# Kernel optimization log

Measured on AMD Instinct MI355X. Metric: run time of the kernel, lower is better.

The kernel has to match this reference:

```python
import jax, jax.numpy as jnp
import numpy as np

AH, AW = 7, 7                # aligned_height, aligned_width
SPATIAL_SCALE = 0.0625       # 1/16


def setup_inputs() -> dict:
    key = jax.random.key(0)
    k1, k2, k3, k4 = jax.random.split(key, 4)
    B, C, H, W = 4, 1024, 64, 64
    N = 2048
    IMG = 1024.0  # image size in pixels; IMG * SPATIAL_SCALE == W
    features = jax.random.normal(k1, (B, C, H, W), dtype=jnp.float32)
    bidx = jax.random.randint(k2, (N,), 0, B).astype(jnp.float32)
    xy1 = jax.random.uniform(k3, (N, 2), minval=0.0, maxval=IMG * 0.7)
    wh = jax.random.uniform(k4, (N, 2), minval=16.0, maxval=IMG * 0.3)
    xy2 = jnp.minimum(xy1 + wh, IMG - 1.0)
    rois = jnp.concatenate(
        [bidx[:, None], xy1[:, 0:1], xy1[:, 1:2], xy2[:, 0:1], xy2[:, 1:2]], axis=1
    ).astype(jnp.float32)
    return {"features": features, "rois": rois}


def reference(features, rois):
    # Faithful port of jwyang's roi_align_kernel (1 sample per bin, inclusive
    # endpoint grid: bin_size = roi_extent / (aligned - 1)).
    B, C, H, W = features.shape
    N = rois.shape[0]
    dt = features.dtype

    batch_ind = rois[:, 0].astype(jnp.int32)                      # [N]
    x1 = rois[:, 1] * SPATIAL_SCALE
    y1 = rois[:, 2] * SPATIAL_SCALE
    x2 = rois[:, 3] * SPATIAL_SCALE
    y2 = rois[:, 4] * SPATIAL_SCALE

    roi_w = jnp.maximum(x2 - x1, 0.0)
    roi_h = jnp.maximum(y2 - y1, 0.0)
    bin_w = roi_w / (AW - 1.0)
    bin_h = roi_h / (AH - 1.0)

    ph = jnp.arange(AH, dtype=dt)
    pw = jnp.arange(AW, dtype=dt)
    h = y1[:, None] + ph[None, :] * bin_h[:, None]                # [N, AH]
    w = x1[:, None] + pw[None, :] * bin_w[:, None]                # [N, AW]

    hstart = jnp.minimum(jnp.floor(h), H - 2.0)                   # [N, AH]
    wstart = jnp.minimum(jnp.floor(w), W - 2.0)                   # [N, AW]
    h_ratio = h - hstart                                          # [N, AH]
    w_ratio = w - wstart                                          # [N, AW]

    # Kernel zeroes out-of-bounds samples.
    valid = ((h >= 0) & (h < H))[:, :, None] & ((w >= 0) & (w < W))[:, None, :]

    hs = jnp.clip(hstart.astype(jnp.int32), 0, H - 2)             # safe gather idx
    ws = jnp.clip(wstart.astype(jnp.int32), 0, W - 2)

    b = batch_ind[:, None, None]                                  # [N,1,1]
    hi = hs[:, :, None]                                           # [N,AH,1]
    wi = ws[:, None, :]                                           # [N,1,AW]

    def gather(dh, dw):
        # mixed advanced indexing -> [N, AH, AW, C]
        return features[b, :, hi + dh, wi + dw]

    ul, ur = gather(0, 0), gather(0, 1)
    dl, dr = gather(1, 0), gather(1, 1)

    hr = h_ratio[:, :, None, None]                                # [N,AH,1,1]
    wr = w_ratio[:, None, :, None]                                # [N,1,AW,1]
    out = (ul * (1 - hr) * (1 - wr) + ur * (1 - hr) * wr
           + dl * hr * (1 - wr) + dr * hr * wr)                   # [N,AH,AW,C]
    out = jnp.where(valid[..., None], out, 0.0)
    return jnp.transpose(out, (0, 3, 1, 2))                       # [N,C,AH,AW]
```

## Files before the change

kernel.cpp:

```cpp
#include <hip/hip_runtime.h>


#define SCALE    0.0625f
#define C_       1024
#define H_       64
#define W_       64
#define HW       (H_ * W_)
#define CHW      (C_ * HW)
#define AH_      7
#define AW_      7
#define NBIN     49
#define PER_ROI  (C_ * NBIN)
#define QCH      32
#define NSLICE   (C_ / QCH)
#define CHUNK    8
#define RCAP     14
#define QCAP     8
#define CSPAN    36
#define NXCD     8

__global__ __launch_bounds__(256, 8) void roialign_kernel(
    const float* __restrict__ feat,
    const float* __restrict__ rois,
    float* __restrict__ out,
    int N)
{
    __shared__ __align__(16) float s_data[CHUNK][RCAP * CSPAN];
    __shared__ float4 s_w[NBIN];
    __shared__ int    s_hs[NBIN], s_ws[NBIN];
    __shared__ int    s_ul[NBIN], s_dl[NBIN];
    __shared__ int    s_goff[NBIN];
    __shared__ int    s_rowG[RCAP];
    __shared__ int    s_quadG[16];
    __shared__ int    s_R, s_Q, s_b;

    const unsigned bidx = blockIdx.x;
    const int xcd       = (int)(bidx & (NXCD - 1));
    const unsigned tmp  = bidx >> 3;
    const int roi       = (int)(tmp % (unsigned)N);
    const int slice_sub = (int)(tmp / (unsigned)N);
    const int slice     = slice_sub * NXCD + xcd;
    const int t = threadIdx.x;

    unsigned long long rm = 0ull;
    unsigned int       qm = 0u;

    if (t < 64) {
        int hs = 0, ws = 0;
        if (t < NBIN) {
            #pragma clang fp contract(off)
            const float r0 = rois[roi * 5 + 0];
            const float r1 = rois[roi * 5 + 1];
            const float r2 = rois[roi * 5 + 2];
            const float r3 = rois[roi * 5 + 3];
            const float r4 = rois[roi * 5 + 4];
            const int   b  = (int)r0;
            const float x1 = r1 * SCALE;
            const float y1 = r2 * SCALE;
            const float x2 = r3 * SCALE;
            const float y2 = r4 * SCALE;
            const float roi_w = fmaxf(x2 - x1, 0.0f);
            const float roi_h = fmaxf(y2 - y1, 0.0f);
            const float bin_w = roi_w / (float)(AW_ - 1);
            const float bin_h = roi_h / (float)(AH_ - 1);

            const int ph = t / AW_;
            const int pw = t - ph * AW_;

            const float h = y1 + (float)ph * bin_h;
            const float w = x1 + (float)pw * bin_w;

            const float hstart = fminf(floorf(h), (float)(H_ - 2));
            const float wstart = fminf(floorf(w), (float)(W_ - 2));
            const float hr = h - hstart;
            const float wr = w - wstart;

            const bool valid = (h >= 0.0f) && (h < (float)H_) &&
                               (w >= 0.0f) && (w < (float)W_);

            hs = min(max((int)hstart, 0), H_ - 2);
            ws = min(max((int)wstart, 0), W_ - 2);

            float wul = (1.0f - hr) * (1.0f - wr);
            float wur = (1.0f - hr) * wr;
            float wdl = hr * (1.0f - wr);
            float wdr = hr * wr;
            if (!valid) { wul = 0.0f; wur = 0.0f; wdl = 0.0f; wdr = 0.0f; }

            s_w[t]    = make_float4(wul, wur, wdl, wdr);
            s_hs[t]   = hs;
            s_ws[t]   = ws;
            s_goff[t] = hs * W_ + ws;
            if (t == 0) s_b = b;

            rm = 3ull << hs;
            qm = (1u << (ws >> 2)) | (1u << ((ws + 1) >> 2));
        }

        #pragma unroll
        for (int d = 1; d < 64; d <<= 1) {
            rm |= __shfl_xor(rm, d);
            qm |= __shfl_xor(qm, d);
        }

        if ((rm >> t) & 1ull)
            s_rowG[__popcll(rm & ((1ull << t) - 1ull))] = t;
        if (t < 16 && ((qm >> t) & 1u))
            s_quadG[__popc(qm & ((1u << t) - 1u))] = t;
        if (t == 0) { s_R = (int)__popcll(rm); s_Q = __popc(qm); }

        if (t < NBIN) {
            const int colIdx = 4 * __popc(qm & ((1u << (ws >> 2)) - 1u)) + (ws & 3);
            const int rsu = __popcll(rm & ((1ull << hs) - 1ull));
            const int rsd = __popcll(rm & ((2ull << hs) - 1ull));
            s_ul[t] = rsu * CSPAN + colIdx;
            s_dl[t] = rsd * CSPAN + colIdx;
        }
    }
    __syncthreads();

    const int R  = s_R;
    const int Qn = s_Q;
    const int rq = R * Qn;

    const float* featC = feat + (size_t)s_b * CHW + (size_t)(slice * QCH) * HW;
    float*       ob    = out + (size_t)roi * PER_ROI + (size_t)(slice * QCH) * NBIN;

    if (Qn > QCAP || R > RCAP) {
        for (int e = t; e < QCH * NBIN; e += 256) {
            const unsigned eu  = (unsigned)e;
            const unsigned c   = eu / NBIN;
            const unsigned bin = eu - c * NBIN;
            const float4 wg  = s_w[bin];
            const int    off = s_goff[bin] + (int)(c << 12);
            const float ul = featC[off];
            const float ur = featC[off + 1];
            const float dl = featC[off + W_];
            const float dr = featC[off + W_ + 1];
            const float v = ul * wg.x + ur * wg.y + dl * wg.z + dr * wg.w;
            __builtin_nontemporal_store(v, ob + e);
        }
        return;
    }

    const int chSpan = 256 / rq;
    const int subCh  = t / rq;
    const int idx    = t % rq;
    const bool loadActive = (subCh < chSpan);
    int gOffT = 0, lOffT = 0;
    if (loadActive) {
        const int r_  = idx / Qn;
        const int sq_ = idx - r_ * Qn;
        gOffT = s_rowG[r_] * W_ + s_quadG[sq_] * 4;
        lOffT = r_ * CSPAN + sq_ * 4;
    }

    const int cl0 = t / NBIN;
    const int bin = t - cl0 * NBIN;
    const bool computeActive = (t < 5 * NBIN);
    float4 w4 = make_float4(0.f, 0.f, 0.f, 0.f);
    int ulo = 0, dlo = 0;
    if (computeActive) { w4 = s_w[bin]; ulo = s_ul[bin]; dlo = s_dl[bin]; }

    for (int cc = 0; cc < QCH; cc += CHUNK) {
        if (loadActive) {
            for (int ch = subCh; ch < CHUNK; ch += chSpan) {
                const float4 v = *(const float4*)(featC + (cc + ch) * HW + gOffT);
                *(float4*)(&s_data[ch][lOffT]) = v;
            }
        }
        __syncthreads();

        if (computeActive) {
            for (int cl = cl0; cl < CHUNK; cl += 5) {
                const float* sd = s_data[cl];
                const float vul = sd[ulo];
                const float vur = sd[ulo + 1];
                const float vdl = sd[dlo];
                const float vdr = sd[dlo + 1];
                const float v = vul * w4.x + vur * w4.y + vdl * w4.z + vdr * w4.w;
                __builtin_nontemporal_store(v, ob + (cc + cl) * NBIN + bin);
            }
        }
        __syncthreads();
    }
}

extern "C" void kernel_launch(void* const* d_in, const int* in_sizes, int n_in,
                              void* d_out, int out_size, void* d_ws, size_t ws_size,
                              hipStream_t stream) {
    const float* feat = (const float*)d_in[0];
    const float* rois = (const float*)d_in[1];
    float* out = (float*)d_out;
    const int N = in_sizes[1] / 5;
    dim3 grid((unsigned)N * NSLICE);
    dim3 block(256);
    roialign_kernel<<<grid, block, 0, stream>>>(feat, rois, out, N);
}
```

Measured before the change: 578.9 us.

## Prefetch next channel chunk into registers and swizzle shared-memory tile layout

Flattens the tile load so every thread issues up to four float4 loads per chunk of channels. The global loads for the next chunk go into registers while the current chunk is interpolated from shared memory, and are written to LDS after a barrier. The LDS layout changes to fixed 32-float rows with an XOR swizzle of quad index by row, with all four corner offsets precomputed per bin. The aim is to hide global-load latency behind compute and cut LDS bank conflicts, at the cost of more registers and an extra barrier per chunk.

```diff
diff --git a/kernel.cpp b/kernel.cpp
--- a/kernel.cpp
+++ b/kernel.cpp
@@ -16,7 +16,7 @@
 #define CHUNK    8
 #define RCAP     14
 #define QCAP     8
-#define CSPAN    36
+#define TILE     456
 #define NXCD     8
 
 __global__ __launch_bounds__(256, 8) void roialign_kernel(
@@ -25,10 +25,9 @@
     float* __restrict__ out,
     int N)
 {
-    __shared__ __align__(16) float s_data[CHUNK][RCAP * CSPAN];
+    __shared__ __align__(16) float s_data[CHUNK * TILE];
     __shared__ float4 s_w[NBIN];
-    __shared__ int    s_hs[NBIN], s_ws[NBIN];
-    __shared__ int    s_ul[NBIN], s_dl[NBIN];
+    __shared__ int4   s_o[NBIN];
     __shared__ int    s_goff[NBIN];
     __shared__ int    s_rowG[RCAP];
     __shared__ int    s_quadG[16];
@@ -88,8 +87,6 @@
             if (!valid) { wul = 0.0f; wur = 0.0f; wdl = 0.0f; wdr = 0.0f; }
 
             s_w[t]    = make_float4(wul, wur, wdl, wdr);
-            s_hs[t]   = hs;
-            s_ws[t]   = ws;
             s_goff[t] = hs * W_ + ws;
             if (t == 0) s_b = b;
 
@@ -110,11 +107,18 @@
         if (t == 0) { s_R = (int)__popcll(rm); s_Q = __popc(qm); }
 
         if (t < NBIN) {
-            const int colIdx = 4 * __popc(qm & ((1u << (ws >> 2)) - 1u)) + (ws & 3);
             const int rsu = __popcll(rm & ((1ull << hs) - 1ull));
             const int rsd = __popcll(rm & ((2ull << hs) - 1ull));
-            s_ul[t] = rsu * CSPAN + colIdx;
-            s_dl[t] = rsd * CSPAN + colIdx;
+            const int w1  = ws + 1;
+            const int sq0 = __popc(qm & ((1u << (ws >> 2)) - 1u));
+            const int sq1 = __popc(qm & ((1u << (w1 >> 2)) - 1u));
+            const int e0  = ws & 3;
+            const int e1  = w1 & 3;
+            s_o[t] = make_int4(
+                rsu * 32 + ((sq0 ^ (rsu & 7)) << 2) + e0,
+                rsu * 32 + ((sq1 ^ (rsu & 7)) << 2) + e1,
+                rsd * 32 + ((sq0 ^ (rsd & 7)) << 2) + e0,
+                rsd * 32 + ((sq1 ^ (rsd & 7)) << 2) + e1);
         }
     }
     __syncthreads();
@@ -143,44 +147,73 @@
         return;
     }
 
-    const int chSpan = 256 / rq;
-    const int subCh  = t / rq;
-    const int idx    = t % rq;
-    const bool loadActive = (subCh < chSpan);
-    int gOffT = 0, lOffT = 0;
-    if (loadActive) {
-        const int r_  = idx / Qn;
-        const int sq_ = idx - r_ * Qn;
-        gOffT = s_rowG[r_] * W_ + s_quadG[sq_] * 4;
-        lOffT = r_ * CSPAN + sq_ * 4;
+    const int rqC = rq * CHUNK;
+    int  gOffA[4], lOffA[4];
+    bool actA[4];
+    #pragma unroll
+    for (int i = 0; i < 4; ++i) {
+        const int j = t + 256 * i;
+        actA[i] = (j < rqC);
+        int g = 0, l = 0;
+        if (actA[i]) {
+            const int ch  = j / rq;
+            const int idx = j - ch * rq;
+            const int r_  = idx / Qn;
+            const int sq  = idx - r_ * Qn;
+            const int qq  = sq ^ (r_ & 7);
+            g = ch * HW + s_rowG[r_] * W_ + s_quadG[sq] * 4;
+            l = ch * TILE + r_ * 32 + qq * 4;
+        }
+        gOffA[i] = g; lOffA[i] = l;
     }
 
     const int cl0 = t / NBIN;
     const int bin = t - cl0 * NBIN;
     const bool computeActive = (t < 5 * NBIN);
     float4 w4 = make_float4(0.f, 0.f, 0.f, 0.f);
-    int ulo = 0, dlo = 0;
-    if (computeActive) { w4 = s_w[bin]; ulo = s_ul[bin]; dlo = s_dl[bin]; }
+    int4   oo = make_int4(0, 0, 0, 0);
+    if (computeActive) { w4 = s_w[bin]; oo = s_o[bin]; }
+
+    float4 pf[4];
+    #pragma unroll
+    for (int i = 0; i < 4; ++i)
+        if (actA[i]) pf[i] = *(const float4*)(featC + gOffA[i]);
+    #pragma unroll
+    for (int i = 0; i < 4; ++i)
+        if (actA[i]) *(float4*)(&s_data[lOffA[i]]) = pf[i];
+    __syncthreads();
 
     for (int cc = 0; cc < QCH; cc += CHUNK) {
-        if (loadActive) {
-            for (int ch = subCh; ch < CHUNK; ch += chSpan) {
-                const float4 v = *(const float4*)(featC + (cc + ch) * HW + gOffT);
-                *(float4*)(&s_data[ch][lOffT]) = v;
+        const bool more = (cc + CHUNK) < QCH;
+
+        if (more) {
+            const float* src = featC + (size_t)(cc + CHUNK) * HW;
+            #pragma unroll
+            for (int i = 0; i < 4; ++i)
+                if (actA[i]) pf[i] = *(const float4*)(src + gOffA[i]);
+        }
+
+        if (computeActive) {
+            #pragma unroll
+            for (int k = 0; k < 2; ++k) {
+                const int cl = cl0 + 5 * k;
+                if (cl < CHUNK) {
+                    const float* tb = s_data + cl * TILE;
+                    const float vul = tb[oo.x];
+                    const float vur = tb[oo.y];
+                    const float vdl = tb[oo.z];
+                    const float vdr = tb[oo.w];
+                    const float v = vul * w4.x + vur * w4.y + vdl * w4.z + vdr * w4.w;
+                    __builtin_nontemporal_store(v, ob + (cc + cl) * NBIN + bin);
+                }
             }
         }
         __syncthreads();
 
-        if (computeActive) {
-            for (int cl = cl0; cl < CHUNK; cl += 5) {
-                const float* sd = s_data[cl];
-                const float vul = sd[ulo];
-                const float vur = sd[ulo + 1];
-                const float vdl = sd[dlo];
-                const float vdr = sd[dlo + 1];
-                const float v = vul * w4.x + vur * w4.y + vdl * w4.z + vdr * w4.w;
-                __builtin_nontemporal_store(v, ob + (cc + cl) * NBIN + bin);
-            }
+        if (more) {
+            #pragma unroll
+            for (int i = 0; i < 4; ++i)
+                if (actA[i]) *(float4*)(&s_data[lOffA[i]]) = pf[i];
         }
         __syncthreads();
     }
```

New measurement: 818.1 us. +41.3%, slower.
